# Performance work log

Measured on AMD Instinct MI355X. Metric: run time of the kernel, lower is better.

## Reference

```python
import jax, jax.numpy as jnp
import numpy as np

NYRS = 8192
PI = np.pi
MMAX, MMIN = 0.76, 0.01
ALPH, M_TH, MU_TH = 0.093, 4.886, 5.8
ROOTD = 1000.0
I0, IF = 1, 12
M0 = 0.2

NDAYS = np.array([0, 31, 28, 31, 30, 31, 30, 31, 31, 30, 31, 30, 31], dtype=np.float64)
CDAYS = np.cumsum(NDAYS).astype(np.int64)


def _insolation_factors(phi):
    """Static (numpy) day-length factors L[12] and insolation response gE[12].
    phi is a non-differentiated scalar latitude in degrees."""
    latr = phi * PI / 180.0
    jday = np.arange(1, 366, dtype=np.float64)
    sd = np.arcsin(np.sin(PI * 23.5 / 180.0) * np.sin(PI * (jday - 80.0) / 180.0))
    y = np.clip(-np.tan(latr) * np.tan(sd), -1.0, 1.0)
    hdl = np.arccos(y)
    dtsi = hdl * np.sin(latr) * np.sin(sd) + np.cos(latr) * np.cos(sd) * np.sin(hdl)
    ndl = dtsi / dtsi.max()
    jday_mid = CDAYS[:-1] + 0.5 * NDAYS[1:]
    m_star = np.clip(1.0 - np.tan(latr) * np.tan(23.439 * PI / 180.0 * np.cos(jday_mid * PI / 182.625)), 0.0, 2.0)
    nhrs = 24.0 * np.arccos(1.0 - m_star) / PI
    L = NDAYS[1:] / 30.0 * (nhrs / 12.0)  # (12,)
    gE = np.array([ndl[CDAYS[t]:CDAYS[t + 1]].mean() for t in range(12)])  # (12,)
    return L.astype(np.float32), gE.astype(np.float32)


def setup_inputs() -> dict:
    key = jax.random.key(0)
    kT, kP = jax.random.split(key)
    T = 10.0 + 8.0 * jax.random.normal(kT, (NYRS, 12), dtype=jnp.float32)   # degC
    P = 100.0 * jax.random.uniform(kP, (NYRS, 12), dtype=jnp.float32)       # mm/month
    return {
        "syear": 0,
        "eyear": NYRS - 1,
        "phi": 45,
        "T": T,
        "P": P,
        "T1": jnp.float32(8.0),
        "T2": jnp.float32(23.0),
        "M1": jnp.float32(0.01),
        "M2": jnp.float32(0.05),
    }


def reference(syear, eyear, phi, T, P, T1, T2, M1, M2):
    nyrs = eyear - syear + 1
    L_np, gE_np = _insolation_factors(float(phi))
    L = jnp.asarray(L_np)        # (12,)
    gE = jnp.asarray(gE_np)      # (12,)

    Tm = T.T                     # (12, nyrs), month-major like torch code
    Pm = P.T                     # (12, nyrs)

    # ---- potential evapotranspiration (Thornthwaite), vectorized over all months ----
    istar = jnp.maximum(Tm / 5.0, 0.0)
    I = jnp.sum(istar ** 1.514, axis=0)                                   # (nyrs,) heat index
    a = 6.75e-07 * I ** 3 - 7.71e-05 * I ** 2 + 0.0179 * I + 0.49         # (nyrs,)
    Tsafe = jnp.clip(Tm, 0.0, 26.5)                                       # avoid neg-base pow
    Ep_mid = 16.0 * L[:, None] * (10.0 * Tsafe / I[None, :]) ** a[None, :]
    Ep_hot = -415.85 + 32.25 * Tm - 0.43 * Tm ** 2
    potEv = jnp.where(Tm < 0.0, 0.0, jnp.where(Tm < 26.5, Ep_mid, Ep_hot))  # (12, nyrs)

    # ---- leaky-bucket soil-moisture recurrence over the 12*nyrs month chain ----
    Pseq = P.reshape(-1)            # year-major month order (matches M[t,y] chain)
    Epseq = potEv.T.reshape(-1)

    def step(prevM, inp):
        p, ep = inp
        Etrans = ep * prevM * ROOTD / (MMAX * ROOTD)
        G = MU_TH * ALPH / (1.0 + MU_TH) * prevM * ROOTD
        R = p * (prevM * ROOTD / (MMAX * ROOTD)) ** M_TH + ALPH / (1.0 + MU_TH) * prevM * ROOTD
        dWdt = p - Etrans - R - G
        newM = jnp.clip(prevM + dWdt / ROOTD, MMIN, MMAX)
        return newM, newM

    _, Mseq = jax.lax.scan(step, jnp.float32(M0), (Pseq, Epseq))
    M = Mseq.reshape(nyrs, 12).T                                           # (12, nyrs)

    # ---- growth responses ----
    gT = jnp.clip((Tm - T1) / (T2 - T1), 0.0, 1.0)
    gM = jnp.clip((M - M1) / (M2 - M1), 0.0, 1.0)
    Gr = jnp.minimum(gT, gM) * gE[:, None]                                 # (12, nyrs)

    # phi > 0 and I_0 = 1 > 0  ->  width[y] = sum Gr[I0-1:IF, y]
    width = jnp.sum(Gr[I0 - 1:IF, :], axis=0)                              # (nyrs,)
    trw = (width - jnp.mean(width)) / jnp.std(width, ddof=1)               # torch.std is unbiased
    return trw
```

## Files before the change

### kernel.cpp

```cpp
#include <hip/hip_runtime.h>
#include <math.h>

#define PI_D 3.14159265358979323846
#define WARM_Y 12
#define BY 256
#define NGRP (BY + WARM_Y)
#define NPAD (NGRP * 13)

#if __has_builtin(__builtin_amdgcn_logf) && __has_builtin(__builtin_amdgcn_exp2f)
__device__ __forceinline__ float flog2(float x) { return __builtin_amdgcn_logf(x); }
__device__ __forceinline__ float fexp2(float x) { return __builtin_amdgcn_exp2f(x); }
#else
__device__ __forceinline__ float flog2(float x) { return log2f(x); }
__device__ __forceinline__ float fexp2(float x) { return exp2f(x); }
#endif
__device__ __forceinline__ float fpow(float x, float y) { return fexp2(y * flog2(x)); }

__constant__ int    c_CDAYS[13] = {0,31,59,90,120,151,181,212,243,273,304,334,365};
__constant__ double c_NDAYS[13] = {0,31,28,31,30,31,30,31,31,30,31,30,31};

__global__ void k_insol(const int* __restrict__ phi_ptr, float* __restrict__ LgE) {
    __shared__ double dtsi_s[365];
    __shared__ double red[64];
    __shared__ double maxd_s;
    const int t = threadIdx.x;
    const double latr = (double)(*phi_ptr) * PI_D / 180.0;
    if (t < 365) {
        double jday = (double)(t + 1);
        double sd = asin(sin(PI_D * 23.5 / 180.0) * sin(PI_D * (jday - 80.0) / 180.0));
        double y = -tan(latr) * tan(sd);
        y = fmin(1.0, fmax(-1.0, y));
        double hdl = acos(y);
        dtsi_s[t] = hdl * sin(latr) * sin(sd) + cos(latr) * cos(sd) * sin(hdl);
    }
    __syncthreads();
    if (t < 64) {
        double mx = -1e300;
        for (int i = t; i < 365; i += 64) mx = fmax(mx, dtsi_s[i]);
        red[t] = mx;
    }
    __syncthreads();
    if (t == 0) {
        double mx = red[0];
        for (int i = 1; i < 64; ++i) mx = fmax(mx, red[i]);
        maxd_s = mx;
    }
    __syncthreads();
    if (t < 12) {
        const int c0 = c_CDAYS[t], c1 = c_CDAYS[t + 1];
        double s = 0.0;
        for (int i = c0; i < c1; ++i) s += dtsi_s[i];
        double gE = (s / (double)(c1 - c0)) / maxd_s;
        double jm = (double)c0 + 0.5 * c_NDAYS[t + 1];
        double ms = 1.0 - tan(latr) * tan(23.439 * PI_D / 180.0 * cos(jm * PI_D / 182.625));
        ms = fmin(2.0, fmax(0.0, ms));
        double nhrs = 24.0 * acos(1.0 - ms) / PI_D;
        double L = c_NDAYS[t + 1] / 30.0 * (nhrs / 12.0);
        LgE[t] = (float)L;
        LgE[12 + t] = (float)gE;
    }
}

__global__ void k_pet(const float* __restrict__ T, const float* __restrict__ LgE,
                      float* __restrict__ A, int nyrs) {
    int y = blockIdx.x * blockDim.x + threadIdx.x;
    if (y >= nyrs) return;
    float Tv[12];
    {
        const float4* T4 = (const float4*)(T + y * 12);
        float4 a = T4[0], b = T4[1], c = T4[2];
        Tv[0]=a.x; Tv[1]=a.y; Tv[2]=a.z; Tv[3]=a.w;
        Tv[4]=b.x; Tv[5]=b.y; Tv[6]=b.z; Tv[7]=b.w;
        Tv[8]=c.x; Tv[9]=c.y; Tv[10]=c.z; Tv[11]=c.w;
    }
    float I = 0.f;
#pragma unroll
    for (int m = 0; m < 12; ++m) {
        float is = fmaxf(Tv[m] * 0.2f, 0.f);
        I += fpow(is, 1.514f);
    }
    float a = 6.75e-07f * I * I * I - 7.71e-05f * I * I + 0.0179f * I + 0.49f;
    float rI = 10.0f / I;
    float Av[12];
#pragma unroll
    for (int m = 0; m < 12; ++m) {
        float t = Tv[m];
        float ep;
        if (t < 0.f) {
            ep = 0.f;
        } else if (t < 26.5f) {
            ep = 16.f * LgE[m] * fpow(t * rI, a);
        } else {
            ep = -415.85f + 32.25f * t - 0.43f * t * t;
        }
        Av[m] = (1.0f - 0.093f) - ep * (1.0f / 760.0f);
    }
    float4* A4 = (float4*)(A + y * 12);
    A4[0] = make_float4(Av[0], Av[1], Av[2], Av[3]);
    A4[1] = make_float4(Av[4], Av[5], Av[6], Av[7]);
    A4[2] = make_float4(Av[8], Av[9], Av[10], Av[11]);
}

__global__ void k_scan(const float* __restrict__ T, const float* __restrict__ P,
                       const float* __restrict__ A, const float* __restrict__ LgE,
                       const float* __restrict__ T1p, const float* __restrict__ T2p,
                       const float* __restrict__ M1p, const float* __restrict__ M2p,
                       float* __restrict__ width, int nyrs) {
    __shared__ float sA[NPAD];
    __shared__ float sB[NPAD];
    __shared__ float sT[NPAD];
    __shared__ float sGE[12];
    const int nmon = nyrs * 12;
    const int base = (blockIdx.x * BY - WARM_Y) * 12;

    for (int t = threadIdx.x; t < NGRP * 12; t += BY) {
        int tg = base + t;
        int pt = t + t / 12;
        float a = 1.0f, p = 0.0f, tt = 0.0f;
        if (tg >= 0 && tg < nmon) { a = A[tg]; p = P[tg]; tt = T[tg]; }
        sA[pt] = a;
        sB[pt] = p * 1e-3f;
        sT[pt] = tt;
    }
    if (threadIdx.x < 12) sGE[threadIdx.x] = LgE[12 + threadIdx.x];
    __syncthreads();

    const int ly = threadIdx.x;
    const int y = blockIdx.x * BY + ly;
    if (y >= nyrs) return;

    const float T1 = *T1p, T2 = *T2p, M1 = *M1p, M2 = *M2p;
    const float invT = 1.0f / (T2 - T1);
    const float invM = 1.0f / (M2 - M1);

    float M = 0.2f;
    int g0 = (blockIdx.x == 0) ? (ly < WARM_Y ? WARM_Y : ly) : ly;

    for (int g = g0; g < ly + WARM_Y; ++g) {
        int pt = g * 13;
#pragma unroll
        for (int m = 0; m < 12; ++m) {
            float a = sA[pt + m], b = sB[pt + m];
            float frac = M * (1.0f / 0.76f);
            float pw = fexp2(4.886f * flog2(frac));
            float K = fmaf(a, M, b);
            M = fmaf(-b, pw, K);
            M = fminf(0.76f, fmaxf(0.01f, M));
        }
    }
    {
        int pt = (ly + WARM_Y) * 13;
        float acc = 0.f;
#pragma unroll
        for (int m = 0; m < 12; ++m) {
            float a = sA[pt + m], b = sB[pt + m];
            float frac = M * (1.0f / 0.76f);
            float pw = fexp2(4.886f * flog2(frac));
            float K = fmaf(a, M, b);
            M = fmaf(-b, pw, K);
            M = fminf(0.76f, fmaxf(0.01f, M));
            float gT = fminf(fmaxf((sT[pt + m] - T1) * invT, 0.f), 1.f);
            float gM = fminf(fmaxf((M - M1) * invM, 0.f), 1.f);
            acc += fminf(gT, gM) * sGE[m];
        }
        width[y] = acc;
    }
}

__global__ void k_norm(const float* __restrict__ width, float* __restrict__ out, int n) {
    __shared__ double s_sum[256];
    __shared__ double s_sq[256];
    __shared__ float mean_s, inv_s;
    const int t = threadIdx.x;
    double sm = 0.0, sq = 0.0;
    for (int i = t; i < n; i += 256) {
        double w = (double)width[i];
        sm += w; sq += w * w;
    }
    s_sum[t] = sm; s_sq[t] = sq;
    __syncthreads();
    for (int off = 128; off > 0; off >>= 1) {
        if (t < off) { s_sum[t] += s_sum[t + off]; s_sq[t] += s_sq[t + off]; }
        __syncthreads();
    }
    if (t == 0) {
        double mean = s_sum[0] / (double)n;
        double var = (s_sq[0] - (double)n * mean * mean) / (double)(n - 1);
        mean_s = (float)mean;
        inv_s = (float)(1.0 / sqrt(var));
    }
    __syncthreads();
    for (int i = t; i < n; i += 256) {
        out[i] = (width[i] - mean_s) * inv_s;
    }
}

extern "C" void kernel_launch(void* const* d_in, const int* in_sizes, int n_in,
                              void* d_out, int out_size, void* d_ws, size_t ws_size,
                              hipStream_t stream) {
    const int*   phi = (const int*)d_in[2];
    const float* T   = (const float*)d_in[3];
    const float* P   = (const float*)d_in[4];
    const float* T1  = (const float*)d_in[5];
    const float* T2  = (const float*)d_in[6];
    const float* M1  = (const float*)d_in[7];
    const float* M2  = (const float*)d_in[8];
    float* out = (float*)d_out;

    const int nyrs = in_sizes[3] / 12;
    const int nmon = nyrs * 12;

    float* ws    = (float*)d_ws;
    float* LgE   = ws;
    float* A     = ws + 32;
    float* width = ws + 32 + nmon;

    k_insol<<<1, 384, 0, stream>>>(phi, LgE);
    k_pet<<<(nyrs + 255) / 256, 256, 0, stream>>>(T, LgE, A, nyrs);
    k_scan<<<(nyrs + BY - 1) / BY, BY, 0, stream>>>(T, P, A, LgE, T1, T2, M1, M2, width, nyrs);
    k_norm<<<1, 256, 0, stream>>>(width, out, nyrs);
}
```

Before: 100.7 us.

## Fuse insolation, PET and scan into one kernel with smaller blocks

Merges the insolation, potential-evapotranspiration and moisture-scan kernels into one kernel. Each block recomputes the day-length and insolation factors in single precision and computes PET for its year window directly into shared memory, so the intermediate A array never goes to global memory and two launches are dropped. Block size drops from 256 to 64 years, giving 128 blocks, and the power term folds the 1/0.76 scale into an additive log constant. The cost is that every block redoes the 365-day insolation work and PET for the warm-up years, and float instead of double for insolation may shift accuracy slightly.

```diff
diff --git a/kernel.cpp b/kernel.cpp
--- a/kernel.cpp
+++ b/kernel.cpp
@@ -1,9 +1,10 @@
 #include <hip/hip_runtime.h>
 #include <math.h>
 
-#define PI_D 3.14159265358979323846
+#define PI_F 3.14159265358979323846f
 #define WARM_Y 12
-#define BY 256
+#define BY 64
+#define BS 64
 #define NGRP (BY + WARM_Y)
 #define NPAD (NGRP * 13)
 
@@ -16,120 +17,101 @@
 #endif
 __device__ __forceinline__ float fpow(float x, float y) { return fexp2(y * flog2(x)); }
 
-__constant__ int    c_CDAYS[13] = {0,31,59,90,120,151,181,212,243,273,304,334,365};
-__constant__ double c_NDAYS[13] = {0,31,28,31,30,31,30,31,31,30,31,30,31};
+__constant__ int   c_CDAYS[13]  = {0,31,59,90,120,151,181,212,243,273,304,334,365};
+__constant__ float c_NDAYSF[13] = {0,31,28,31,30,31,30,31,31,30,31,30,31};
 
-__global__ void k_insol(const int* __restrict__ phi_ptr, float* __restrict__ LgE) {
-    __shared__ double dtsi_s[365];
-    __shared__ double red[64];
-    __shared__ double maxd_s;
-    const int t = threadIdx.x;
-    const double latr = (double)(*phi_ptr) * PI_D / 180.0;
-    if (t < 365) {
-        double jday = (double)(t + 1);
-        double sd = asin(sin(PI_D * 23.5 / 180.0) * sin(PI_D * (jday - 80.0) / 180.0));
-        double y = -tan(latr) * tan(sd);
-        y = fmin(1.0, fmax(-1.0, y));
-        double hdl = acos(y);
-        dtsi_s[t] = hdl * sin(latr) * sin(sd) + cos(latr) * cos(sd) * sin(hdl);
-    }
-    __syncthreads();
-    if (t < 64) {
-        double mx = -1e300;
-        for (int i = t; i < 365; i += 64) mx = fmax(mx, dtsi_s[i]);
-        red[t] = mx;
-    }
-    __syncthreads();
-    if (t == 0) {
-        double mx = red[0];
-        for (int i = 1; i < 64; ++i) mx = fmax(mx, red[i]);
-        maxd_s = mx;
-    }
-    __syncthreads();
-    if (t < 12) {
-        const int c0 = c_CDAYS[t], c1 = c_CDAYS[t + 1];
-        double s = 0.0;
-        for (int i = c0; i < c1; ++i) s += dtsi_s[i];
-        double gE = (s / (double)(c1 - c0)) / maxd_s;
-        double jm = (double)c0 + 0.5 * c_NDAYS[t + 1];
-        double ms = 1.0 - tan(latr) * tan(23.439 * PI_D / 180.0 * cos(jm * PI_D / 182.625));
-        ms = fmin(2.0, fmax(0.0, ms));
-        double nhrs = 24.0 * acos(1.0 - ms) / PI_D;
-        double L = c_NDAYS[t + 1] / 30.0 * (nhrs / 12.0);
-        LgE[t] = (float)L;
-        LgE[12 + t] = (float)gE;
-    }
-}
+#define POW_C 1.9345076f
 
-__global__ void k_pet(const float* __restrict__ T, const float* __restrict__ LgE,
-                      float* __restrict__ A, int nyrs) {
-    int y = blockIdx.x * blockDim.x + threadIdx.x;
-    if (y >= nyrs) return;
-    float Tv[12];
-    {
-        const float4* T4 = (const float4*)(T + y * 12);
-        float4 a = T4[0], b = T4[1], c = T4[2];
-        Tv[0]=a.x; Tv[1]=a.y; Tv[2]=a.z; Tv[3]=a.w;
-        Tv[4]=b.x; Tv[5]=b.y; Tv[6]=b.z; Tv[7]=b.w;
-        Tv[8]=c.x; Tv[9]=c.y; Tv[10]=c.z; Tv[11]=c.w;
-    }
-    float I = 0.f;
-#pragma unroll
-    for (int m = 0; m < 12; ++m) {
-        float is = fmaxf(Tv[m] * 0.2f, 0.f);
-        I += fpow(is, 1.514f);
-    }
-    float a = 6.75e-07f * I * I * I - 7.71e-05f * I * I + 0.0179f * I + 0.49f;
-    float rI = 10.0f / I;
-    float Av[12];
-#pragma unroll
-    for (int m = 0; m < 12; ++m) {
-        float t = Tv[m];
-        float ep;
-        if (t < 0.f) {
-            ep = 0.f;
-        } else if (t < 26.5f) {
-            ep = 16.f * LgE[m] * fpow(t * rI, a);
-        } else {
-            ep = -415.85f + 32.25f * t - 0.43f * t * t;
-        }
-        Av[m] = (1.0f - 0.093f) - ep * (1.0f / 760.0f);
-    }
-    float4* A4 = (float4*)(A + y * 12);
-    A4[0] = make_float4(Av[0], Av[1], Av[2], Av[3]);
-    A4[1] = make_float4(Av[4], Av[5], Av[6], Av[7]);
-    A4[2] = make_float4(Av[8], Av[9], Av[10], Av[11]);
-}
-
-__global__ void k_scan(const float* __restrict__ T, const float* __restrict__ P,
-                       const float* __restrict__ A, const float* __restrict__ LgE,
-                       const float* __restrict__ T1p, const float* __restrict__ T2p,
-                       const float* __restrict__ M1p, const float* __restrict__ M2p,
-                       float* __restrict__ width, int nyrs) {
+__global__ void k_fused(const int* __restrict__ phi_ptr,
+                        const float* __restrict__ T, const float* __restrict__ P,
+                        const float* __restrict__ T1p, const float* __restrict__ T2p,
+                        const float* __restrict__ M1p, const float* __restrict__ M2p,
+                        float* __restrict__ width, int nyrs) {
     __shared__ float sA[NPAD];
     __shared__ float sB[NPAD];
     __shared__ float sT[NPAD];
-    __shared__ float sGE[12];
+    __shared__ float dtsi[365];
+    __shared__ float sL[12], sGE[12];
+    __shared__ float maxd;
+
+    const int tid = threadIdx.x;
+    const float latr = (float)(*phi_ptr) * (PI_F / 180.f);
+    const float tl = tanf(latr), slat = sinf(latr), clat = cosf(latr);
+    const float T1 = *T1p, T2 = *T2p, M1 = *M1p, M2 = *M2p;
+
+    for (int d = tid; d < 365; d += BS) {
+        float jd = (float)(d + 1);
+        float sd = asinf(sinf(PI_F * 23.5f / 180.f) * sinf(PI_F * (jd - 80.f) / 180.f));
+        float y  = fminf(1.f, fmaxf(-1.f, -tl * tanf(sd)));
+        float hdl = acosf(y);
+        dtsi[d] = hdl * slat * sinf(sd) + clat * cosf(sd) * sinf(hdl);
+    }
+
     const int nmon = nyrs * 12;
     const int base = (blockIdx.x * BY - WARM_Y) * 12;
-
-    for (int t = threadIdx.x; t < NGRP * 12; t += BY) {
+    for (int t = tid; t < NGRP * 12; t += BS) {
         int tg = base + t;
         int pt = t + t / 12;
-        float a = 1.0f, p = 0.0f, tt = 0.0f;
-        if (tg >= 0 && tg < nmon) { a = A[tg]; p = P[tg]; tt = T[tg]; }
-        sA[pt] = a;
+        float p = 0.f, tt = 0.f;
+        if (tg >= 0 && tg < nmon) { p = P[tg]; tt = T[tg]; }
         sB[pt] = p * 1e-3f;
         sT[pt] = tt;
     }
-    if (threadIdx.x < 12) sGE[threadIdx.x] = LgE[12 + threadIdx.x];
     __syncthreads();
 
-    const int ly = threadIdx.x;
+    {
+        float mx = -1e30f;
+        for (int i = tid; i < 365; i += BS) mx = fmaxf(mx, dtsi[i]);
+        for (int off = 32; off > 0; off >>= 1) mx = fmaxf(mx, __shfl_down(mx, off));
+        if (tid == 0) maxd = mx;
+    }
+    __syncthreads();
+
+    if (tid < 12) {
+        int c0 = c_CDAYS[tid], c1 = c_CDAYS[tid + 1];
+        float s = 0.f;
+        for (int i = c0; i < c1; ++i) s += dtsi[i];
+        sGE[tid] = (s / (float)(c1 - c0)) / maxd;
+        float nd = c_NDAYSF[tid + 1];
+        float jm = (float)c0 + 0.5f * nd;
+        float ms = 1.f - tl * tanf(23.439f * PI_F / 180.f * cosf(jm * PI_F / 182.625f));
+        ms = fminf(2.f, fmaxf(0.f, ms));
+        float nhrs = 24.f * acosf(1.f - ms) / PI_F;
+        sL[tid] = nd / 30.f * (nhrs / 12.f);
+    }
+    __syncthreads();
+
+    for (int g = tid; g < NGRP; g += BS) {
+        int yg = blockIdx.x * BY - WARM_Y + g;
+        int pt = g * 13;
+        if (yg < 0 || yg >= nyrs) {
+#pragma unroll
+            for (int m = 0; m < 12; ++m) sA[pt + m] = 1.f;
+            continue;
+        }
+        float I = 0.f;
+#pragma unroll
+        for (int m = 0; m < 12; ++m) {
+            float is = fmaxf(sT[pt + m] * 0.2f, 0.f);
+            I += fpow(is, 1.514f);
+        }
+        float a  = 6.75e-07f * I * I * I - 7.71e-05f * I * I + 0.0179f * I + 0.49f;
+        float rI = 10.0f / I;
+#pragma unroll
+        for (int m = 0; m < 12; ++m) {
+            float t = sT[pt + m];
+            float ep;
+            if (t < 0.f)          ep = 0.f;
+            else if (t < 26.5f)   ep = 16.f * sL[m] * fpow(t * rI, a);
+            else                  ep = -415.85f + 32.25f * t - 0.43f * t * t;
+            sA[pt + m] = (1.0f - 0.093f) - ep * (1.0f / 760.0f);
+        }
+    }
+    __syncthreads();
+
+    const int ly = tid;
     const int y = blockIdx.x * BY + ly;
     if (y >= nyrs) return;
-
-    const float T1 = *T1p, T2 = *T2p, M1 = *M1p, M2 = *M2p;
     const float invT = 1.0f / (T2 - T1);
     const float invM = 1.0f / (M2 - M1);
 
@@ -141,8 +123,7 @@
 #pragma unroll
         for (int m = 0; m < 12; ++m) {
             float a = sA[pt + m], b = sB[pt + m];
-            float frac = M * (1.0f / 0.76f);
-            float pw = fexp2(4.886f * flog2(frac));
+            float pw = fexp2(fmaf(4.886f, flog2(M), POW_C));
             float K = fmaf(a, M, b);
             M = fmaf(-b, pw, K);
             M = fminf(0.76f, fmaxf(0.01f, M));
@@ -154,8 +135,7 @@
 #pragma unroll
         for (int m = 0; m < 12; ++m) {
             float a = sA[pt + m], b = sB[pt + m];
-            float frac = M * (1.0f / 0.76f);
-            float pw = fexp2(4.886f * flog2(frac));
+            float pw = fexp2(fmaf(4.886f, flog2(M), POW_C));
             float K = fmaf(a, M, b);
             M = fmaf(-b, pw, K);
             M = fminf(0.76f, fmaxf(0.01f, M));
@@ -167,14 +147,14 @@
     }
 }
 
-__global__ void k_norm(const float* __restrict__ width, float* __restrict__ out, int n) {
+__global__ void k_norm(float* __restrict__ out, int n) {
     __shared__ double s_sum[256];
     __shared__ double s_sq[256];
     __shared__ float mean_s, inv_s;
     const int t = threadIdx.x;
     double sm = 0.0, sq = 0.0;
     for (int i = t; i < n; i += 256) {
-        double w = (double)width[i];
+        double w = (double)out[i];
         sm += w; sq += w * w;
     }
     s_sum[t] = sm; s_sq[t] = sq;
@@ -191,7 +171,7 @@
     }
     __syncthreads();
     for (int i = t; i < n; i += 256) {
-        out[i] = (width[i] - mean_s) * inv_s;
+        out[i] = (out[i] - mean_s) * inv_s;
     }
 }
 
@@ -208,15 +188,7 @@
     float* out = (float*)d_out;
 
     const int nyrs = in_sizes[3] / 12;
-    const int nmon = nyrs * 12;
 
-    float* ws    = (float*)d_ws;
-    float* LgE   = ws;
-    float* A     = ws + 32;
-    float* width = ws + 32 + nmon;
-
-    k_insol<<<1, 384, 0, stream>>>(phi, LgE);
-    k_pet<<<(nyrs + 255) / 256, 256, 0, stream>>>(T, LgE, A, nyrs);
-    k_scan<<<(nyrs + BY - 1) / BY, BY, 0, stream>>>(T, P, A, LgE, T1, T2, M1, M2, width, nyrs);
-    k_norm<<<1, 256, 0, stream>>>(width, out, nyrs);
+    k_fused<<<(nyrs + BY - 1) / BY, BS, 0, stream>>>(phi, T, P, T1, T2, M1, M2, out, nyrs);
+    k_norm<<<1, 256, 0, stream>>>(out, nyrs);
 }
```

New measurement: 98.18 us. 1.03x faster.
